# Optimization experiments

Measured on AMD Instinct MI355X. Metric: run time of the kernel, lower is better.

## Reference

```python
import math
import jax, jax.numpy as jnp
import numpy as np

B, T, D, H, FACTOR = 8, 4096, 1024, 16, 5
DH = D // H


def setup_inputs() -> dict:
    key = jax.random.key(0)
    ks = jax.random.split(key, 7)
    u = max(1, min(int(FACTOR * math.log(T + 1)), T))  # = 41
    s = 1.0 / np.sqrt(D).astype(np.float32)
    x = jax.random.normal(ks[0], (B, T, D), jnp.float32)
    Wq = jax.random.normal(ks[1], (D, D), jnp.float32) * s
    Wk = jax.random.normal(ks[2], (D, D), jnp.float32) * s
    Wv = jax.random.normal(ks[3], (D, D), jnp.float32) * s
    Wo = jax.random.normal(ks[4], (D, D), jnp.float32) * s
    bo = jax.random.normal(ks[5], (D,), jnp.float32) * 0.01
    # unique indices, mirroring torch.randperm(T)[:u]
    idx = jax.random.permutation(ks[6], T)[:u].astype(jnp.int32)
    return {"x": x, "Wq": Wq, "Wk": Wk, "Wv": Wv, "Wo": Wo, "bo": bo, "idx": idx}


def reference(x, Wq, Wk, Wv, Wo, bo, idx):
    Bx, Tx, Dx = x.shape
    scale = 1.0 / np.sqrt(DH).astype(np.float32)

    def proj(W):  # torch Linear: x @ W.T, then split heads -> [B,H,T,Dh]
        return (x @ W.T).reshape(Bx, Tx, H, DH).transpose(0, 2, 1, 3)

    Q = proj(Wq)
    K = proj(Wk)
    V = proj(Wv)

    Qs = Q[:, :, idx, :]                                   # [B,H,u,Dh] gather
    scores = jnp.einsum('bhud,bhtd->bhut', Qs, K) * scale  # [B,H,u,T]
    attn = jax.nn.softmax(scores, axis=-1)
    ctx = jnp.einsum('bhut,bhtd->bhud', attn, V)           # [B,H,u,Dh]

    # mean over the u sampled positions fills non-sampled slots
    out = jnp.broadcast_to(ctx.mean(axis=2, keepdims=True), (Bx, H, Tx, DH))
    out = out.at[:, :, idx, :].set(ctx)                    # scatter ctx back

    y = out.transpose(0, 2, 1, 3).reshape(Bx, Tx, Dx)
    return y @ Wo.T + bo
```

## Files before the change

### kernel.cpp

```cpp
#include <hip/hip_runtime.h>
#include <hip/hip_bf16.h>

#define B_  8
#define T_  4096
#define D_  1024
#define H_  16
#define DH_ 64
#define NC_ 4

typedef __bf16 bf8 __attribute__((ext_vector_type(8)));
typedef float f32x4 __attribute__((ext_vector_type(4)));

__device__ __forceinline__ unsigned short f2bf_rn(float f) {
    unsigned u = __float_as_uint(f);
    unsigned r = (u + 0x7FFF + ((u >> 16) & 1)) >> 16;
    return (unsigned short)r;
}

__device__ __forceinline__ void async_load16(const void* gp, void* lp) {
    __builtin_amdgcn_global_load_lds(
        (const __attribute__((address_space(1))) unsigned*)(gp),
        (__attribute__((address_space(3))) unsigned*)(lp), 16, 0, 0);
}


__global__ void k_sel(const int* __restrict__ idx, int* __restrict__ sel, int U) {
    for (int t = threadIdx.x; t < T_; t += 256) sel[t] = 0;
    __syncthreads();
    if (threadIdx.x < U) sel[idx[threadIdx.x]] = threadIdx.x + 1;
}

__global__ void k_gather(const float* __restrict__ x, const int* __restrict__ idx,
                         float* __restrict__ xs, int U) {
    int bi = blockIdx.x;
    int b = bi / U, i = bi - b * U;
    int t = idx[i];
    const float4* src = (const float4*)(x + ((size_t)(b * T_ + t)) * D_);
    float4* dst = (float4*)(xs + (size_t)bi * D_);
    dst[threadIdx.x] = src[threadIdx.x];
}

__global__ void k_cvt_flat(const float* __restrict__ src, short* __restrict__ dst) {
    size_t i = ((size_t)blockIdx.x * 256 + threadIdx.x) * 8;
    float4 a = *(const float4*)(src + i);
    float4 b = *(const float4*)(src + i + 4);
    short4 s0, s1;
    s0.x = (short)f2bf_rn(a.x); s0.y = (short)f2bf_rn(a.y);
    s0.z = (short)f2bf_rn(a.z); s0.w = (short)f2bf_rn(a.w);
    s1.x = (short)f2bf_rn(b.x); s1.y = (short)f2bf_rn(b.y);
    s1.z = (short)f2bf_rn(b.z); s1.w = (short)f2bf_rn(b.w);
    *(short4*)(dst + i) = s0;
    *(short4*)(dst + i + 4) = s1;
}

__global__ void k_zpad(short* __restrict__ Qtb, int HU, int MP) {
    int bi = blockIdx.x;
    int npad = MP - HU;
    int b = bi / npad, r = bi - b * npad;
    short4 z = {0, 0, 0, 0};
    *(short4*)(Qtb + ((size_t)b * MP + HU + r) * D_ + threadIdx.x * 4) = z;
}

__global__ __launch_bounds__(256) void k_proj(const float* __restrict__ A,
                                              const float* __restrict__ W,
                                              const float* __restrict__ bias,
                                              float* __restrict__ C, int M) {
    __shared__ float As[32][64 + 4];
    __shared__ float Bs[32][64 + 4];
    int m0 = blockIdx.x * 64, n0 = blockIdx.y * 64;
    int tid = threadIdx.x;
    int lr = tid >> 3;
    int lc = (tid & 7) * 4;
    int ty = tid >> 4, tx = tid & 15;
    float acc[4][4] = {{0.f}};
    for (int k0 = 0; k0 < D_; k0 += 32) {
#pragma unroll
        for (int half = 0; half < 2; ++half) {
            int r = lr + half * 32;
            int gm = m0 + r;
            float4 v = make_float4(0.f, 0.f, 0.f, 0.f);
            if (gm < M) v = *(const float4*)(A + (size_t)gm * D_ + k0 + lc);
            As[lc + 0][r] = v.x; As[lc + 1][r] = v.y; As[lc + 2][r] = v.z; As[lc + 3][r] = v.w;
            int gn = n0 + r;
            float4 w = *(const float4*)(W + (size_t)gn * D_ + k0 + lc);
            Bs[lc + 0][r] = w.x; Bs[lc + 1][r] = w.y; Bs[lc + 2][r] = w.z; Bs[lc + 3][r] = w.w;
        }
        __syncthreads();
#pragma unroll
        for (int kk = 0; kk < 32; ++kk) {
            float4 a = *(const float4*)&As[kk][ty * 4];
            float4 bb = *(const float4*)&Bs[kk][tx * 4];
            acc[0][0] += a.x * bb.x; acc[0][1] += a.x * bb.y; acc[0][2] += a.x * bb.z; acc[0][3] += a.x * bb.w;
            acc[1][0] += a.y * bb.x; acc[1][1] += a.y * bb.y; acc[1][2] += a.y * bb.z; acc[1][3] += a.y * bb.w;
            acc[2][0] += a.z * bb.x; acc[2][1] += a.z * bb.y; acc[2][2] += a.z * bb.z; acc[2][3] += a.z * bb.w;
            acc[3][0] += a.w * bb.x; acc[3][1] += a.w * bb.y; acc[3][2] += a.w * bb.z; acc[3][3] += a.w * bb.w;
        }
        __syncthreads();
    }
#pragma unroll
    for (int i = 0; i < 4; ++i) {
        int gm = m0 + ty * 4 + i;
        if (gm < M) {
            int gn = n0 + tx * 4;
            float4 v = make_float4(acc[i][0], acc[i][1], acc[i][2], acc[i][3]);
            if (bias) {
                v.x += bias[gn + 0]; v.y += bias[gn + 1];
                v.z += bias[gn + 2]; v.w += bias[gn + 3];
            }
            *(float4*)(C + (size_t)gm * D_ + gn) = v;
        }
    }
}

__global__ __launch_bounds__(256) void k_qth(const float* __restrict__ Qs,
                                             const float* __restrict__ Wk,
                                             short* __restrict__ Qtb, int U, int MP) {
    __shared__ float As[32][64 + 4];
    __shared__ float Bs[32][64 + 4];
    int h = blockIdx.z;
    int m0 = blockIdx.x * 64, n0 = blockIdx.y * 64;
    int BU = B_ * U;
    int tid = threadIdx.x;
    int lr = tid >> 3, lc = (tid & 7) * 4;
    int ty = tid >> 4, tx = tid & 15;
    float acc[4][4] = {{0.f}};
    for (int k0 = 0; k0 < DH_; k0 += 32) {
#pragma unroll
        for (int half = 0; half < 2; ++half) {
            int r = lr + half * 32;
            int gm = m0 + r;
            float4 v = make_float4(0.f, 0.f, 0.f, 0.f);
            if (gm < BU) v = *(const float4*)(Qs + (size_t)gm * D_ + h * DH_ + k0 + lc);
            As[lc + 0][r] = v.x; As[lc + 1][r] = v.y; As[lc + 2][r] = v.z; As[lc + 3][r] = v.w;
            int kr = (tid >> 4) + half * 16;
            int nc = (tid & 15) * 4;
            float4 w = *(const float4*)(Wk + ((size_t)(h * DH_ + k0 + kr)) * D_ + n0 + nc);
            *(float4*)&Bs[kr][nc] = w;
        }
        __syncthreads();
#pragma unroll
        for (int kk = 0; kk < 32; ++kk) {
            float4 a = *(const float4*)&As[kk][ty * 4];
            float4 bb = *(const float4*)&Bs[kk][tx * 4];
            acc[0][0] += a.x * bb.x; acc[0][1] += a.x * bb.y; acc[0][2] += a.x * bb.z; acc[0][3] += a.x * bb.w;
            acc[1][0] += a.y * bb.x; acc[1][1] += a.y * bb.y; acc[1][2] += a.y * bb.z; acc[1][3] += a.y * bb.w;
            acc[2][0] += a.z * bb.x; acc[2][1] += a.z * bb.y; acc[2][2] += a.z * bb.z; acc[2][3] += a.z * bb.w;
            acc[3][0] += a.w * bb.x; acc[3][1] += a.w * bb.y; acc[3][2] += a.w * bb.z; acc[3][3] += a.w * bb.w;
        }
        __syncthreads();
    }
#pragma unroll
    for (int i = 0; i < 4; ++i) {
        int gm = m0 + ty * 4 + i;
        if (gm < BU) {
            int b = gm / U, ii = gm - b * U;
            short4 s;
            s.x = (short)f2bf_rn(0.125f * acc[i][0]);
            s.y = (short)f2bf_rn(0.125f * acc[i][1]);
            s.z = (short)f2bf_rn(0.125f * acc[i][2]);
            s.w = (short)f2bf_rn(0.125f * acc[i][3]);
            *(short4*)(Qtb + ((size_t)b * MP + h * U + ii) * D_ + n0 + tx * 4) = s;
        }
    }
}

#define GEMM_NT 16

__device__ __forceinline__ void stage64(const short* __restrict__ Ag,
                                        const short* __restrict__ Bg,
                                        short* lA, short* lB, int kt, int tid) {
#pragma unroll
    for (int i = 0; i < 4; ++i) {
        int li = i * 512 + tid;
        int row = li >> 3, sl = li & 7;
        int off = row * D_ + kt + ((sl ^ (row & 7)) << 3);
        async_load16(Ag + off, lA + li * 8);
        async_load16(Bg + off, lB + li * 8);
    }
}

__device__ __forceinline__ bf8 lds_frag(const short* l, int R, int slot) {
    return *(const bf8*)(l + R * 64 + (((slot) ^ (R & 7)) << 3));
}

__device__ __forceinline__ void gemm256_core(const short* __restrict__ Ag,
                                             const short* __restrict__ Bg,
                                             short* lA0, short* lB0,
                                             f32x4 (&acc)[8][4]) {
    int tid = threadIdx.x;
    int lane = tid & 63, w = tid >> 6;
    int wr = w >> 2, wc = w & 3;
    int ln = lane & 15, q = lane >> 4;
#pragma unroll
    for (int mi = 0; mi < 8; ++mi)
#pragma unroll
        for (int ni = 0; ni < 4; ++ni)
            acc[mi][ni] = (f32x4){0.f, 0.f, 0.f, 0.f};

    stage64(Ag, Bg, lA0, lB0, 0, tid);
    stage64(Ag, Bg, lA0 + 16384, lB0 + 16384, 64, tid);

#pragma unroll 1
    for (int t = 0; t < GEMM_NT; ++t) {
        const int p = t & 1;
        short* lA = lA0 + p * 16384;
        short* lB = lB0 + p * 16384;
        if (t < GEMM_NT - 1) asm volatile("s_waitcnt vmcnt(8)" ::: "memory");
        else                 asm volatile("s_waitcnt vmcnt(0)" ::: "memory");
        __builtin_amdgcn_s_barrier();

        bf8 bfrag[4][2], afrag[4][2];
#pragma unroll
        for (int ni = 0; ni < 4; ++ni)
#pragma unroll
            for (int kh = 0; kh < 2; ++kh)
                bfrag[ni][kh] = lds_frag(lB, wc * 64 + ni * 16 + ln, kh * 4 + q);
#pragma unroll
        for (int mi = 0; mi < 4; ++mi)
#pragma unroll
            for (int kh = 0; kh < 2; ++kh)
                afrag[mi][kh] = lds_frag(lA, wr * 128 + mi * 16 + ln, kh * 4 + q);
        __builtin_amdgcn_s_setprio(1);
#pragma unroll
        for (int kh = 0; kh < 2; ++kh)
#pragma unroll
            for (int mi = 0; mi < 4; ++mi)
#pragma unroll
                for (int ni = 0; ni < 4; ++ni)
                    acc[mi][ni] = __builtin_amdgcn_mfma_f32_16x16x32_bf16(
                        afrag[mi][kh], bfrag[ni][kh], acc[mi][ni], 0, 0, 0);
        __builtin_amdgcn_s_setprio(0);
#pragma unroll
        for (int mi = 0; mi < 4; ++mi)
#pragma unroll
            for (int kh = 0; kh < 2; ++kh)
                afrag[mi][kh] = lds_frag(lA, wr * 128 + 64 + mi * 16 + ln, kh * 4 + q);
        __builtin_amdgcn_s_setprio(1);
#pragma unroll
        for (int kh = 0; kh < 2; ++kh)
#pragma unroll
            for (int mi = 0; mi < 4; ++mi)
#pragma unroll
                for (int ni = 0; ni < 4; ++ni)
                    acc[4 + mi][ni] = __builtin_amdgcn_mfma_f32_16x16x32_bf16(
                        afrag[mi][kh], bfrag[ni][kh], acc[4 + mi][ni], 0, 0, 0);
        __builtin_amdgcn_s_setprio(0);
        asm volatile("" ::: "memory");
        __builtin_amdgcn_s_barrier();
        if (t + 2 < GEMM_NT)
            stage64(Ag, Bg, lA, lB, (t + 2) * 64, tid);
    }
}

__global__ __launch_bounds__(512, 2) void k_scores2(const short* __restrict__ Qtb,
                                                    const short* __restrict__ xb,
                                                    short* __restrict__ attnb, int MP) {
    __shared__ short lA[2][16384];
    __shared__ short lB[2][16384];
    int bid = blockIdx.x;
    int lg = (bid & 7) * (gridDim.x >> 3) + (bid >> 3);
    int MT = MP >> 8;
    int per_b = MT << 4;
    int b = lg / per_b;
    int r = lg - b * per_b;
    int mt = r >> 4, nt = r & 15;
    const short* Ag = Qtb + ((size_t)b * MP + mt * 256) * D_;
    const short* Bg = xb + ((size_t)b * T_ + nt * 256) * D_;
    f32x4 acc[8][4];
    gemm256_core(Ag, Bg, &lA[0][0], &lB[0][0], acc);

    short* Cb = attnb + (size_t)b * MP * T_;
    int tid = threadIdx.x;
    int lane = tid & 63, w = tid >> 6;
    int wr = w >> 2, wc = w & 3;
    int ln = lane & 15, q = lane >> 4;
    int row0 = mt * 256 + wr * 128;
    int col0 = nt * 256 + wc * 64;
#pragma unroll
    for (int mi = 0; mi < 8; ++mi)
#pragma unroll
        for (int ni = 0; ni < 4; ++ni) {
            int col = col0 + ni * 16 + ln;
#pragma unroll
            for (int rr = 0; rr < 4; ++rr) {
                int grow = row0 + mi * 16 + q * 4 + rr;
                Cb[(size_t)grow * T_ + col] = (short)f2bf_rn(__expf(acc[mi][ni][rr]));
            }
        }
}

__global__ __launch_bounds__(512, 2) void k_v2(const short* __restrict__ xb,
                                               const short* __restrict__ Wvb,
                                               short* __restrict__ Vt) {
    __shared__ short lA[2][16384];
    __shared__ short lB[2][16384];
    int bid = blockIdx.x;
    int lg = (bid & 7) * (gridDim.x >> 3) + (bid >> 3);
    int mt = lg >> 2, nt = lg & 3;
    const short* Ag = xb + (size_t)mt * 256 * D_;
    const short* Bg = Wvb + (size_t)nt * 256 * D_;
    f32x4 acc[8][4];
    gemm256_core(Ag, Bg, &lA[0][0], &lB[0][0], acc);

    int tid = threadIdx.x;
    int lane = tid & 63, w = tid >> 6;
    int wr = w >> 2, wc = w & 3;
    int ln = lane & 15, q = lane >> 4;
    int h = nt * 4 + wc;
    int b = mt >> 4;
    int tIn = (mt & 15) * 256 + wr * 128;
    const int PITCH = 136;
    short* ep = &lA[0][0] + w * 2304;
    size_t vbase = ((size_t)(b * H_ + h) * DH_) * T_;
#pragma unroll
    for (int ni = 0; ni < 4; ++ni) {
#pragma unroll
        for (int mi = 0; mi < 8; ++mi) {
            short4 s;
            s.x = (short)f2bf_rn(acc[mi][ni][0]);
            s.y = (short)f2bf_rn(acc[mi][ni][1]);
            s.z = (short)f2bf_rn(acc[mi][ni][2]);
            s.w = (short)f2bf_rn(acc[mi][ni][3]);
            *(short4*)(ep + ln * PITCH + mi * 16 + q * 4) = s;
        }
        __syncthreads();
#pragma unroll
        for (int it = 0; it < 2; ++it) {
            int dhl = it * 8 + (lane >> 3);
            int seg = lane & 7;
            bf8 v0 = *(const bf8*)(ep + dhl * PITCH + seg * 8);
            bf8 v1 = *(const bf8*)(ep + dhl * PITCH + (seg + 8) * 8);
            int dh = ni * 16 + dhl;
            *(bf8*)(Vt + vbase + (size_t)dh * T_ + tIn + seg * 8) = v0;
            *(bf8*)(Vt + vbase + (size_t)dh * T_ + tIn + 64 + seg * 8) = v1;
        }
        __syncthreads();
    }
}

__global__ __launch_bounds__(256) void k_pv(const short* __restrict__ attnb,
                                            const short* __restrict__ Vt,
                                            float* __restrict__ Op,
                                            float* __restrict__ rsp,
                                            int U, int MP) {
    __shared__ short vt[64 * 136];
    __shared__ short at[48 * 136];
    int gid = blockIdx.x;
    int c = gid & (NC_ - 1);
    int bh = gid >> 2;
    int h = bh & (H_ - 1);
    int b = bh >> 4;
    int tid = threadIdx.x;
    int lane = tid & 63, w = tid >> 6;
    int quad = lane >> 4;
    const short* Arow = attnb + ((size_t)b * MP + h * U) * T_;
    const short* Vrow = Vt + (size_t)bh * DH_ * T_;

    f32x4 O[3];
#pragma unroll
    for (int mi = 0; mi < 3; ++mi) O[mi] = (f32x4){0.f, 0.f, 0.f, 0.f};
    float rs[3] = {0.f, 0.f, 0.f};

    for (int tt = 0; tt < (T_ / NC_) / 128; ++tt) {
        int t0 = c * (T_ / NC_) + tt * 128;
#pragma unroll
        for (int it = 0; it < 4; ++it) {
            int idx = it * 256 + tid;
            int dh = idx >> 4, seg = idx & 15;
            bf8 v = *(const bf8*)(Vrow + (size_t)dh * T_ + t0 + seg * 8);
            *(bf8*)(vt + dh * 136 + seg * 8) = v;
        }
#pragma unroll
        for (int it = 0; it < 3; ++it) {
            int idx = it * 256 + tid;
            int r = idx >> 4, seg = idx & 15;
            bf8 v = *(const bf8*)(Arow + (size_t)r * T_ + t0 + seg * 8);
            *(bf8*)(at + r * 136 + seg * 8) = v;
        }
        __syncthreads();
        bf8 af[3][4];
#pragma unroll
        for (int mi = 0; mi < 3; ++mi)
#pragma unroll
            for (int kf = 0; kf < 4; ++kf)
                af[mi][kf] = *(const bf8*)(at + (mi * 16 + (lane & 15)) * 136 + kf * 32 + quad * 8);
        if (w == 0) {
#pragma unroll
            for (int mi = 0; mi < 3; ++mi)
#pragma unroll
                for (int kf = 0; kf < 4; ++kf)
#pragma unroll
                    for (int j = 0; j < 8; ++j) rs[mi] += (float)af[mi][kf][j];
        }
#pragma unroll
        for (int kf = 0; kf < 4; ++kf) {
            bf8 bfr = *(const bf8*)(vt + (w * 16 + (lane & 15)) * 136 + kf * 32 + quad * 8);
#pragma unroll
            for (int mi = 0; mi < 3; ++mi)
                O[mi] = __builtin_amdgcn_mfma_f32_16x16x32_bf16(af[mi][kf], bfr, O[mi], 0, 0, 0);
        }
        __syncthreads();
    }
#pragma unroll
    for (int mi = 0; mi < 3; ++mi)
#pragma unroll
        for (int r = 0; r < 4; ++r)
            Op[((size_t)gid * 48 + mi * 16 + quad * 4 + r) * DH_ + w * 16 + (lane & 15)] = O[mi][r];
    if (w == 0) {
#pragma unroll
        for (int mi = 0; mi < 3; ++mi) {
            rs[mi] += __shfl_xor(rs[mi], 16);
            rs[mi] += __shfl_xor(rs[mi], 32);
            if (quad == 0) rsp[(size_t)gid * 48 + mi * 16 + lane] = rs[mi];
        }
    }
}

__global__ __launch_bounds__(256) void k_rows2(const float* __restrict__ Op,
                                               const float* __restrict__ rsp,
                                               float* __restrict__ R, int U) {
    __shared__ float inv[48];
    __shared__ float msum[4][64];
    int bh = blockIdx.x;
    int b = bh >> 4, h = bh & (H_ - 1);
    int tid = threadIdx.x;
    if (tid < 48) {
        float s = 0.f;
        for (int cc = 0; cc < NC_; ++cc) s += rsp[(size_t)(bh * NC_ + cc) * 48 + tid];
        inv[tid] = 1.f / s;
    }
    __syncthreads();
    int dh = tid & 63, ig = tid >> 6;
    float acc = 0.f;
    for (int p = 0; p < 11; ++p) {
        int i = p * 4 + ig;
        if (i < U) {
            float o = 0.f;
            for (int cc = 0; cc < NC_; ++cc)
                o += Op[((size_t)(bh * NC_ + cc) * 48 + i) * DH_ + dh];
            float v = o * inv[i];
            R[((size_t)b * (U + 1) + 1 + i) * D_ + h * DH_ + dh] = v;
            acc += v;
        }
    }
    msum[ig][dh] = acc;
    __syncthreads();
    if (ig == 0)
        R[((size_t)b * (U + 1)) * D_ + h * DH_ + dh] =
            (msum[0][dh] + msum[1][dh] + msum[2][dh] + msum[3][dh]) / (float)U;
}

__global__ __launch_bounds__(256) void k_fill(const float* __restrict__ Yr,
                                              const int* __restrict__ sel,
                                              float* __restrict__ y, int U) {
    int blk = blockIdx.x;
    int b = blk >> 12, t = blk & (T_ - 1);
    int j = sel[t];
    const float4* src = (const float4*)(Yr + ((size_t)b * (U + 1) + j) * D_);
    float4* dst = (float4*)(y + (size_t)blk * D_);
    dst[threadIdx.x] = src[threadIdx.x];
}

extern "C" void kernel_launch(void* const* d_in, const int* in_sizes, int n_in,
                              void* d_out, int out_size, void* d_ws, size_t ws_size,
                              hipStream_t stream) {
    const float* x  = (const float*)d_in[0];
    const float* Wq = (const float*)d_in[1];
    const float* Wk = (const float*)d_in[2];
    const float* Wv = (const float*)d_in[3];
    const float* Wo = (const float*)d_in[4];
    const float* bo = (const float*)d_in[5];
    const int*  idx = (const int*)d_in[6];
    int U = in_sizes[6];
    int HU = H_ * U;
    int MP = ((HU + 127) / 128) * 128;

    char* w = (char*)d_ws;
    auto alloc = [&](size_t bytes) { char* p = w; w += (bytes + 255) & ~(size_t)255; return p; };

    float* xs    = (float*)alloc((size_t)B_ * U * D_ * 4);
    float* Qs    = (float*)alloc((size_t)B_ * U * D_ * 4);
    short* Qtb   = (short*)alloc((size_t)B_ * MP * D_ * 2);
    short* xb    = (short*)alloc((size_t)B_ * T_ * D_ * 2);
    short* Wvb   = (short*)alloc((size_t)D_ * D_ * 2);
    short* attnb = (short*)alloc((size_t)B_ * MP * T_ * 2);
    short* Vtb   = (short*)alloc((size_t)B_ * D_ * T_ * 2);
    float* Opb   = (float*)alloc((size_t)B_ * H_ * NC_ * 48 * DH_ * 4);
    float* rspb  = (float*)alloc((size_t)B_ * H_ * NC_ * 48 * 4);
    float* R     = (float*)alloc((size_t)B_ * (U + 1) * D_ * 4);
    float* Yr    = (float*)alloc((size_t)B_ * (U + 1) * D_ * 4);
    int*   sel   = (int*)alloc((size_t)T_ * 4);

    int MT = MP / 256;

    k_sel<<<dim3(1), dim3(256), 0, stream>>>(idx, sel, U);
    k_gather<<<dim3(B_ * U), dim3(256), 0, stream>>>(x, idx, xs, U);
    k_proj<<<dim3((B_ * U + 63) / 64, D_ / 64), dim3(256), 0, stream>>>(xs, Wq, nullptr, Qs, B_ * U);
    k_cvt_flat<<<dim3((size_t)B_ * T_ * D_ / 2048), dim3(256), 0, stream>>>(x, xb);
    k_cvt_flat<<<dim3((size_t)D_ * D_ / 2048), dim3(256), 0, stream>>>(Wv, Wvb);
    k_zpad<<<dim3(B_ * (MP - HU)), dim3(256), 0, stream>>>(Qtb, HU, MP);
    k_qth<<<dim3((B_ * U + 63) / 64, D_ / 64, H_), dim3(256), 0, stream>>>(Qs, Wk, Qtb, U, MP);
    k_scores2<<<dim3(B_ * MT * 16), dim3(512), 0, stream>>>(Qtb, xb, attnb, MP);
    k_v2<<<dim3((B_ * T_ / 256) * (D_ / 256)), dim3(512), 0, stream>>>(xb, Wvb, Vtb);
    k_pv<<<dim3(B_ * H_ * NC_), dim3(256), 0, stream>>>(attnb, Vtb, Opb, rspb, U, MP);
    k_rows2<<<dim3(B_ * H_), dim3(256), 0, stream>>>(Opb, rspb, R, U);
    k_proj<<<dim3((B_ * (U + 1) + 63) / 64, D_ / 64), dim3(256), 0, stream>>>(R, Wo, bo, Yr, B_ * (U + 1));
    k_fill<<<dim3(B_ * T_), dim3(256), 0, stream>>>(Yr, sel, (float*)d_out, U);
}
```

Before: 579.2 us.

## Merge scores and V-projection GEMMs into one launch and drop zero-pad kernel

Fuses the separate scores GEMM and V-projection GEMM kernels into a single k_gemm launch. Block index ranges select which GEMM and epilogue each workgroup runs, so the two under-filled grids share the GPU and their tail waves overlap. The k_zpad launch that zeroed the padding rows of Qtb is removed. This saves a launch but leaves the padded query rows uninitialised, which is safe only if downstream kernels never read those rows. The scores branch hardcodes 48 tiles per batch, tying it to the current MP.

Measured after the change: 566.8 us. 1.02x faster.

```diff
diff --git a/kernel.cpp b/kernel.cpp
--- a/kernel.cpp
+++ b/kernel.cpp
@@ -53,14 +53,6 @@
     *(short4*)(dst + i + 4) = s1;
 }
 
-__global__ void k_zpad(short* __restrict__ Qtb, int HU, int MP) {
-    int bi = blockIdx.x;
-    int npad = MP - HU;
-    int b = bi / npad, r = bi - b * npad;
-    short4 z = {0, 0, 0, 0};
-    *(short4*)(Qtb + ((size_t)b * MP + HU + r) * D_ + threadIdx.x * 4) = z;
-}
-
 __global__ __launch_bounds__(256) void k_proj(const float* __restrict__ A,
                                               const float* __restrict__ W,
                                               const float* __restrict__ bias,
@@ -252,89 +244,77 @@
     }
 }
 
-__global__ __launch_bounds__(512, 2) void k_scores2(const short* __restrict__ Qtb,
-                                                    const short* __restrict__ xb,
-                                                    short* __restrict__ attnb, int MP) {
-    __shared__ short lA[2][16384];
-    __shared__ short lB[2][16384];
+__global__ __launch_bounds__(512, 2) void k_gemm(const short* __restrict__ Qtb,
+                                                 const short* __restrict__ xb,
+                                                 const short* __restrict__ Wvb,
+                                                 short* __restrict__ attnb,
+                                                 short* __restrict__ Vt, int MP) {
+    __shared__ short lAB[4][16384];
     int bid = blockIdx.x;
-    int lg = (bid & 7) * (gridDim.x >> 3) + (bid >> 3);
-    int MT = MP >> 8;
-    int per_b = MT << 4;
-    int b = lg / per_b;
-    int r = lg - b * per_b;
-    int mt = r >> 4, nt = r & 15;
-    const short* Ag = Qtb + ((size_t)b * MP + mt * 256) * D_;
-    const short* Bg = xb + ((size_t)b * T_ + nt * 256) * D_;
-    f32x4 acc[8][4];
-    gemm256_core(Ag, Bg, &lA[0][0], &lB[0][0], acc);
-
-    short* Cb = attnb + (size_t)b * MP * T_;
+    int cpx = gridDim.x >> 3;
+    int lg = (bid & 7) * cpx + (bid >> 3);
     int tid = threadIdx.x;
     int lane = tid & 63, w = tid >> 6;
     int wr = w >> 2, wc = w & 3;
     int ln = lane & 15, q = lane >> 4;
-    int row0 = mt * 256 + wr * 128;
-    int col0 = nt * 256 + wc * 64;
-#pragma unroll
-    for (int mi = 0; mi < 8; ++mi)
+    f32x4 acc[8][4];
+
+    if (lg < 512) {
+        int mt = lg >> 2, nt = lg & 3;
+        gemm256_core(xb + (size_t)mt * 256 * D_, Wvb + (size_t)nt * 256 * D_,
+                     &lAB[0][0], &lAB[2][0], acc);
+        int h = nt * 4 + wc;
+        int b = mt >> 4;
+        int tIn = (mt & 15) * 256 + wr * 128;
+        const int PITCH = 136;
+        short* ep = &lAB[0][0] + w * 2304;
+        size_t vbase = ((size_t)(b * H_ + h) * DH_) * T_;
 #pragma unroll
         for (int ni = 0; ni < 4; ++ni) {
-            int col = col0 + ni * 16 + ln;
-#pragma unroll
-            for (int rr = 0; rr < 4; ++rr) {
-                int grow = row0 + mi * 16 + q * 4 + rr;
-                Cb[(size_t)grow * T_ + col] = (short)f2bf_rn(__expf(acc[mi][ni][rr]));
+#pragma unroll
+            for (int mi = 0; mi < 8; ++mi) {
+                short4 s;
+                s.x = (short)f2bf_rn(acc[mi][ni][0]);
+                s.y = (short)f2bf_rn(acc[mi][ni][1]);
+                s.z = (short)f2bf_rn(acc[mi][ni][2]);
+                s.w = (short)f2bf_rn(acc[mi][ni][3]);
+                *(short4*)(ep + ln * PITCH + mi * 16 + q * 4) = s;
             }
-        }
-}
-
-__global__ __launch_bounds__(512, 2) void k_v2(const short* __restrict__ xb,
-                                               const short* __restrict__ Wvb,
-                                               short* __restrict__ Vt) {
-    __shared__ short lA[2][16384];
-    __shared__ short lB[2][16384];
-    int bid = blockIdx.x;
-    int lg = (bid & 7) * (gridDim.x >> 3) + (bid >> 3);
-    int mt = lg >> 2, nt = lg & 3;
-    const short* Ag = xb + (size_t)mt * 256 * D_;
-    const short* Bg = Wvb + (size_t)nt * 256 * D_;
-    f32x4 acc[8][4];
-    gemm256_core(Ag, Bg, &lA[0][0], &lB[0][0], acc);
-
-    int tid = threadIdx.x;
-    int lane = tid & 63, w = tid >> 6;
-    int wr = w >> 2, wc = w & 3;
-    int ln = lane & 15, q = lane >> 4;
-    int h = nt * 4 + wc;
-    int b = mt >> 4;
-    int tIn = (mt & 15) * 256 + wr * 128;
-    const int PITCH = 136;
-    short* ep = &lA[0][0] + w * 2304;
-    size_t vbase = ((size_t)(b * H_ + h) * DH_) * T_;
-#pragma unroll
-    for (int ni = 0; ni < 4; ++ni) {
-#pragma unroll
-        for (int mi = 0; mi < 8; ++mi) {
-            short4 s;
-            s.x = (short)f2bf_rn(acc[mi][ni][0]);
-            s.y = (short)f2bf_rn(acc[mi][ni][1]);
-            s.z = (short)f2bf_rn(acc[mi][ni][2]);
-            s.w = (short)f2bf_rn(acc[mi][ni][3]);
-            *(short4*)(ep + ln * PITCH + mi * 16 + q * 4) = s;
-        }
-        __syncthreads();
-#pragma unroll
-        for (int it = 0; it < 2; ++it) {
-            int dhl = it * 8 + (lane >> 3);
-            int seg = lane & 7;
-            bf8 v0 = *(const bf8*)(ep + dhl * PITCH + seg * 8);
-            bf8 v1 = *(const bf8*)(ep + dhl * PITCH + (seg + 8) * 8);
-            int dh = ni * 16 + dhl;
-            *(bf8*)(Vt + vbase + (size_t)dh * T_ + tIn + seg * 8) = v0;
-            *(bf8*)(Vt + vbase + (size_t)dh * T_ + tIn + 64 + seg * 8) = v1;
-        }
-        __syncthreads();
+            __syncthreads();
+#pragma unroll
+            for (int it = 0; it < 2; ++it) {
+                int dhl = it * 8 + (lane >> 3);
+                int seg = lane & 7;
+                bf8 v0 = *(const bf8*)(ep + dhl * PITCH + seg * 8);
+                bf8 v1 = *(const bf8*)(ep + dhl * PITCH + (seg + 8) * 8);
+                int dh = ni * 16 + dhl;
+                *(bf8*)(Vt + vbase + (size_t)dh * T_ + tIn + seg * 8) = v0;
+                *(bf8*)(Vt + vbase + (size_t)dh * T_ + tIn + 64 + seg * 8) = v1;
+            }
+            __syncthreads();
+        }
+    } else {
+        int r2 = lg - 512;
+        int b = r2 / 48;
+        int rr = r2 - b * 48;
+        int mt = rr >> 4, nt = rr & 15;
+        gemm256_core(Qtb + ((size_t)b * MP + mt * 256) * D_,
+                     xb + ((size_t)b * T_ + nt * 256) * D_,
+                     &lAB[0][0], &lAB[2][0], acc);
+        short* Cb = attnb + (size_t)b * MP * T_;
+        int row0 = mt * 256 + wr * 128;
+        int col0 = nt * 256 + wc * 64;
+#pragma unroll
+        for (int mi = 0; mi < 8; ++mi)
+#pragma unroll
+            for (int ni = 0; ni < 4; ++ni) {
+                int col = col0 + ni * 16 + ln;
+#pragma unroll
+                for (int rr2 = 0; rr2 < 4; ++rr2) {
+                    int grow = row0 + mi * 16 + q * 4 + rr2;
+                    Cb[(size_t)grow * T_ + col] = (short)f2bf_rn(__expf(acc[mi][ni][rr2]));
+                }
+            }
     }
 }
 
@@ -491,17 +471,13 @@
     float* Yr    = (float*)alloc((size_t)B_ * (U + 1) * D_ * 4);
     int*   sel   = (int*)alloc((size_t)T_ * 4);
 
-    int MT = MP / 256;
-
     k_sel<<<dim3(1), dim3(256), 0, stream>>>(idx, sel, U);
     k_gather<<<dim3(B_ * U), dim3(256), 0, stream>>>(x, idx, xs, U);
     k_proj<<<dim3((B_ * U + 63) / 64, D_ / 64), dim3(256), 0, stream>>>(xs, Wq, nullptr, Qs, B_ * U);
     k_cvt_flat<<<dim3((size_t)B_ * T_ * D_ / 2048), dim3(256), 0, stream>>>(x, xb);
     k_cvt_flat<<<dim3((size_t)D_ * D_ / 2048), dim3(256), 0, stream>>>(Wv, Wvb);
-    k_zpad<<<dim3(B_ * (MP - HU)), dim3(256), 0, stream>>>(Qtb, HU, MP);
     k_qth<<<dim3((B_ * U + 63) / 64, D_ / 64, H_), dim3(256), 0, stream>>>(Qs, Wk, Qtb, U, MP);
-    k_scores2<<<dim3(B_ * MT * 16), dim3(512), 0, stream>>>(Qtb, xb, attnb, MP);
-    k_v2<<<dim3((B_ * T_ / 256) * (D_ / 256)), dim3(512), 0, stream>>>(xb, Wvb, Vtb);
+    k_gemm<<<dim3(512 + B_ * 48), dim3(512), 0, stream>>>(Qtb, xb, Wvb, attnb, Vtb, MP);
     k_pv<<<dim3(B_ * H_ * NC_), dim3(256), 0, stream>>>(attnb, Vtb, Opb, rspb, U, MP);
     k_rows2<<<dim3(B_ * H_), dim3(256), 0, stream>>>(Opb, rspb, R, U);
     k_proj<<<dim3((B_ * (U + 1) + 63) / 64, D_ / 64), dim3(256), 0, stream>>>(R, Wo, bo, Yr, B_ * (U + 1));
```
